# Kernel optimization log

Hardware: AMD Instinct MI355X
Metric: run time of the kernel (lower is better)

Reference implementation:

```python
import jax, jax.numpy as jnp
import numpy as np

T = 2048
D_IN = 1024
D_OUT = 1024
N_HEAD = 16
HEAD_DIM = D_OUT // N_HEAD


def setup_inputs() -> dict:
    key = jax.random.key(0)
    kx, kq, kk, kv = jax.random.split(key, 4)
    s = 1.0 / np.sqrt(D_IN)
    return {
        "x": jax.random.normal(kx, (T, D_IN), dtype=jnp.float32),
        "W_q": jax.random.normal(kq, (D_OUT, D_IN), dtype=jnp.float32) * s,
        "W_k": jax.random.normal(kk, (D_OUT, D_IN), dtype=jnp.float32) * s,
        "W_v": jax.random.normal(kv, (D_OUT, D_IN), dtype=jnp.float32) * s,
    }


def reference(x, W_q, W_k, W_v):
    t = x.shape[0]
    # linear projections (torch Linear: y = x @ W.T), split into heads: [H, T, Dh]
    q = (x @ W_q.T).reshape(t, N_HEAD, HEAD_DIM).transpose(1, 0, 2)
    k = (x @ W_k.T).reshape(t, N_HEAD, HEAD_DIM).transpose(1, 0, 2)
    v = (x @ W_v.T).reshape(t, N_HEAD, HEAD_DIM).transpose(1, 0, 2)
    # raw scores [H, T, T]
    omega = jnp.einsum("hqd,hkd->hqk", q, k)
    causal = jnp.triu(jnp.ones((t, t), dtype=bool), k=1)
    omega = jnp.where(causal[None, :, :], -jnp.inf, omega)
    # NOTE: faithful to source quirk — divides by head_dim**(-0.5),
    # i.e. multiplies scores by sqrt(head_dim)
    att_w = jax.nn.softmax(omega * (HEAD_DIM ** 0.5), axis=-1)
    context = jnp.einsum("hqk,hkd->hqd", att_w, v)  # [H, T, Dh]
    return context.transpose(1, 0, 2).reshape(t, D_OUT)
```

## Files before the change

kernel.cpp:

```cpp
#include <hip/hip_runtime.h>
#include <hip/hip_bf16.h>


typedef __bf16 bf16x8 __attribute__((ext_vector_type(8)));
typedef __bf16 bf16x4 __attribute__((ext_vector_type(4)));
typedef float  f32x4  __attribute__((ext_vector_type(4)));
typedef float  f32x16 __attribute__((ext_vector_type(16)));
typedef unsigned int u32;
typedef u32 u32x2 __attribute__((ext_vector_type(2)));
typedef u32 u32x4 __attribute__((ext_vector_type(4)));

#define MFMA(a, b, c) __builtin_amdgcn_mfma_f32_16x16x32_bf16((a), (b), (c), 0, 0, 0)
#define MFMA32(a, b, c) __builtin_amdgcn_mfma_f32_32x32x16_bf16((a), (b), (c), 0, 0, 0)

#if __has_builtin(__builtin_amdgcn_exp2f)
#define EXP2F(x) __builtin_amdgcn_exp2f(x)
#else
#define EXP2F(x) exp2f(x)
#endif

constexpr int T = 2048, DIN = 1024, DOUT = 1024, NH = 16, DH = 64;
constexpr float SC = 11.5415603f;
constexpr float DEFER = 0.6931472f;

constexpr size_t SZ_XMAT = (size_t)T * DIN * 2;
constexpr size_t SZ_WMAT = (size_t)DOUT * DIN * 2;
constexpr size_t OFF_XH = 0;
constexpr size_t OFF_XL = OFF_XH + SZ_XMAT;
constexpr size_t OFF_QH = OFF_XL + SZ_XMAT;
constexpr size_t OFF_QL = OFF_QH + SZ_XMAT;
constexpr size_t OFF_KH = OFF_QL + SZ_XMAT;
constexpr size_t OFF_KL = OFF_KH + SZ_XMAT;
constexpr size_t OFF_VT = OFF_KL + SZ_XMAT;
constexpr size_t OFF_W  = OFF_VT + SZ_XMAT;

__device__ __forceinline__ void gload_lds16(const void* g, void* l) {
  __builtin_amdgcn_global_load_lds(
      (const __attribute__((address_space(1))) void*)g,
      (__attribute__((address_space(3))) void*)l, 16, 0, 0);
}

__device__ __forceinline__ float xor32f(float x, int hi) {
#if __has_builtin(__builtin_amdgcn_permlane32_swap)
  const u32 xu = __builtin_bit_cast(u32, x);
  const u32x2 rp = __builtin_amdgcn_permlane32_swap(xu, xu, false, false);
  return __builtin_bit_cast(float, hi ? rp[0] : rp[1]);
#else
  return __shfl_xor(x, 32, 64);
#endif
}

__global__ void split_all(const float* __restrict__ x, const float* __restrict__ wq,
                          const float* __restrict__ wk, const float* __restrict__ wv,
                          char* __restrict__ ws) {
  const int i = blockIdx.x * 256 + threadIdx.x;
  const float* src;
  __bf16 *hi, *lo;
  int off;
  if (i < T * DIN / 4) {
    src = x; off = i;
    hi = (__bf16*)(ws + OFF_XH);
    lo = (__bf16*)(ws + OFF_XL);
  } else {
    const int j = i - T * DIN / 4;
    const int z = j >> 18;
    off = j & 262143;
    src = (z == 0) ? wq : ((z == 1) ? wk : wv);
    hi = (__bf16*)(ws + OFF_W + (size_t)z * 2 * SZ_WMAT);
    lo = hi + (size_t)DOUT * DIN;
  }
  const f32x4 v = ((const f32x4*)src)[off];
  bf16x4 h, l;
#pragma unroll
  for (int j = 0; j < 4; ++j) {
    const float xv = v[j];
    const __bf16 hh = (__bf16)xv;
    h[j] = hh;
    l[j] = (__bf16)(xv - (float)hh);
  }
  ((bf16x4*)hi)[off] = h;
  ((bf16x4*)lo)[off] = l;
}

__device__ __forceinline__ void proj_loop_qk(const __bf16* __restrict__ Ah,
                                             const __bf16* __restrict__ Al,
                                             const __bf16* __restrict__ Bh,
                                             const __bf16* __restrict__ Bl,
                                             __bf16* lds, int tm, int tn, int lane,
                                             int wv, f32x4 (&acc)[4][4]) {
  constexpr int BUF = 16384, BOFF = 8192;
  const int wm = wv >> 1, wn = wv & 1;
  const int q4 = lane >> 4, r16 = lane & 15;

  auto STAGE = [&](int ks, int buf) {
    const int k0 = ks * 32;
    __bf16* base = lds + buf * BUF;
#pragma unroll
    for (int j = 0; j < 2; ++j) {
      const int cbase = wv * 128 + j * 64;
      const int cidx = cbase + lane;
      const int row = cidx & 127, kc = cidx >> 7;
      const size_t ga = (size_t)(tm + row) * DIN + k0 + kc * 8;
      const size_t gb = (size_t)(tn + row) * DIN + k0 + kc * 8;
      gload_lds16(Ah + ga, base + cbase * 8);
      gload_lds16(Bh + gb, base + BOFF + cbase * 8);
      gload_lds16(Al + ga, base + 4096 + cbase * 8);
      gload_lds16(Bl + gb, base + 12288 + cbase * 8);
    }
  };

  STAGE(0, 0);
  STAGE(1, 1);

  for (int ks = 0; ks < 32; ++ks) {
    const int buf = ks & 1;
    if (ks < 31) asm volatile("s_waitcnt vmcnt(8)" ::: "memory");
    else         asm volatile("s_waitcnt vmcnt(0)" ::: "memory");
// ... 71 lines not shown
        }
  } else {
    const int vt = bid - 256;
    const int tm = (vt >> 3) * 64;
    const int tn = (vt & 7) * 128;
    const __bf16* Bh = (const __bf16*)(ws + OFF_W + 2 * 2 * SZ_WMAT);

    auto STAGE = [&](int ks, int buf) {
      const int k0 = ks * 32;
      __bf16* base = lds + buf * 6144;
      {
        const int cbase = wv * 64;
        const int c = cbase + lane;
        const int row = c & 63, kc = c >> 6;
        gload_lds16(Ah + (size_t)(tm + row) * DIN + k0 + kc * 8, base + cbase * 8);
      }
#pragma unroll
      for (int j = 0; j < 2; ++j) {
        const int cbase = wv * 128 + j * 64;
        const int c = cbase + lane;
        const int row = c & 127, kc = c >> 7;
        gload_lds16(Bh + (size_t)(tn + row) * DIN + k0 + kc * 8,
                    base + 2048 + cbase * 8);
      }
    };

    f32x4 acc[4][2] = {};
    STAGE(0, 0);
    STAGE(1, 1);
    for (int ks = 0; ks < 32; ++ks) {
      const int buf = ks & 1;
      if (ks < 31) asm volatile("s_waitcnt vmcnt(3)" ::: "memory");
      else         asm volatile("s_waitcnt vmcnt(0)" ::: "memory");
      __builtin_amdgcn_s_barrier();
      __builtin_amdgcn_sched_barrier(0);

      const __bf16* ldsA = lds + buf * 6144;
      const __bf16* ldsB = ldsA + 2048;
      bf16x8 fa[4], fb[2];
#pragma unroll
      for (int b = 0; b < 4; ++b)
        fa[b] = *(const bf16x8*)(ldsA + (q4 * 64 + b * 16 + r16) * 8);
#pragma unroll
      for (int b = 0; b < 2; ++b)
        fb[b] = *(const bf16x8*)(ldsB + (q4 * 128 + wv * 32 + b * 16 + r16) * 8);
      __builtin_amdgcn_s_setprio(1);
#pragma unroll
      for (int bm = 0; bm < 4; ++bm)
#pragma unroll
        for (int bn = 0; bn < 2; ++bn)
          acc[bm][bn] = MFMA(fa[bm], fb[bn], acc[bm][bn]);
      __builtin_amdgcn_s_setprio(0);
      asm volatile("s_waitcnt lgkmcnt(0)" ::: "memory");
      __builtin_amdgcn_sched_barrier(0);
      __builtin_amdgcn_s_barrier();
      __builtin_amdgcn_sched_barrier(0);
      if (ks < 30) STAGE(ks + 2, buf);
    }

    __syncthreads();
    __bf16* tb = lds;
#pragma unroll
    for (int bm = 0; bm < 4; ++bm)
#pragma unroll
      for (int bn = 0; bn < 2; ++bn)
#pragma unroll
        for (int r = 0; r < 4; ++r) {
          const int tl = bm * 16 + q4 * 4 + r;
          const int nl = wv * 32 + bn * 16 + r16;
          tb[(size_t)nl * 72 + tl] = (__bf16)acc[bm][bn][r];
        }
    __syncthreads();
    __bf16* Vt = (__bf16*)(ws + OFF_VT);
#pragma unroll
    for (int it = 0; it < 4; ++it) {
      const int cid = it * 256 + tid;
      const int nl = cid >> 3, tc = cid & 7;
      const bf16x8 vd = *(const bf16x8*)(tb + (size_t)nl * 72 + tc * 8);
      *(bf16x8*)(Vt + (size_t)(tn + nl) * T + tm + tc * 8) = vd;
    }
  }
}

__global__ __launch_bounds__(256, 2) void attn_kernel(const char* __restrict__ ws,
                                                      float* __restrict__ out) {
  const int bid = blockIdx.x;
  const int h = bid & 15;
  const int qt = (bid < 256) ? (31 - (bid >> 4)) : ((bid - 256) >> 4);
  const int tid = threadIdx.x;
  const int lane = tid & 63, wid = tid >> 6;
  const int qhalf = wid & 1, kvpar = wid >> 1;
  const int r32 = lane & 31, hi = lane >> 5, hi8 = hi * 8;
  const int qg = qt * 64 + qhalf * 32 + r32;
  const int NT = qt + 1;
  const int mid = (NT + 1) >> 1;
  const int tBeg = kvpar ? mid : 0;
  const int tEnd = kvpar ? NT : mid;

  const __bf16* Qh = (const __bf16*)(ws + OFF_QH);
  const __bf16* Ql = (const __bf16*)(ws + OFF_QL);
  const __bf16* Kh = (const __bf16*)(ws + OFF_KH);
  const __bf16* Kl = (const __bf16*)(ws + OFF_KL);
  const __bf16* Vt = (const __bf16*)(ws + OFF_VT);

  __shared__ alignas(16) __bf16 sK[2][2][2][64 * 72];

  bf16x8 fqh[4], fql[4];
#pragma unroll
  for (int ds = 0; ds < 4; ++ds) {
    const size_t off = (size_t)qg * DOUT + h * 64 + ds * 16 + hi8;
    fqh[ds] = *(const bf16x8*)(Qh + off);
    fql[ds] = *(const bf16x8*)(Ql + off);
  }

  bf16x8 st[8];
  const int hid = qhalf * 64 + lane;
  auto ISSUE = [&](int t) {
    const int kv0 = t * 64;
#pragma unroll
    for (int j = 0; j < 4; ++j) {
      const int c = j * 128 + hid;
      const int row = c >> 3, dc = c & 7;
      const size_t ko = (size_t)(kv0 + row) * DOUT + h * 64 + dc * 8;
      st[j] = *(const bf16x8*)(Kh + ko);
      st[4 + j] = *(const bf16x8*)(Kl + ko);
    }
  };
  auto WRITE = [&](int b) {
#pragma unroll
    for (int j = 0; j < 4; ++j) {
      const int c = j * 128 + hid;
      const int row = c >> 3, dc = c & 7;
      *(bf16x8*)(&sK[kvpar][b][0][row * 72 + dc * 8]) = st[j];
      *(bf16x8*)(&sK[kvpar][b][1][row * 72 + dc * 8]) = st[4 + j];
    }
  };

  f32x16 acc0 = {}, acc1 = {};
  float mrun = -1e30f, lrun = 0.f;

  if (tBeg < tEnd) {
    ISSUE(tBeg);
    WRITE(0);
    if (tBeg + 1 < tEnd) ISSUE(tBeg + 1);
  }
  asm volatile("s_waitcnt lgkmcnt(0)" ::: "memory");
  __builtin_amdgcn_sched_barrier(0);
  __builtin_amdgcn_s_barrier();
  __builtin_amdgcn_sched_barrier(0);

  for (int it = 0; it < mid; ++it) {
    const int t = tBeg + it;
    const int p = it & 1;
    if (t < tEnd) {
      if (t + 1 < tEnd) {
        WRITE(p ^ 1);
        if (t + 2 < tEnd) ISSUE(t + 2);
      }

      const int kv0 = t * 64;
      const bool dodiag = (t == NT - 1);
      const bool do1 = !(dodiag && qhalf == 0);

      bf16x8 va0[4], va1[4];
#pragma unroll
      for (int ks = 0; ks < 4; ++ks) {
        const size_t vo = (size_t)(h * 64 + r32) * T + kv0 + ks * 16 + hi8;
        va0[ks] = *(const bf16x8*)(Vt + vo);
        va1[ks] = *(const bf16x8*)(Vt + vo + (size_t)32 * T);
      }

      const __bf16* kbh = &sK[kvpar][p][0][0];
      const __bf16* kbl = &sK[kvpar][p][1][0];
      f32x16 s0 = {}, s1 = {};
      __builtin_amdgcn_s_setprio(1);
#pragma unroll
      for (int ds = 0; ds < 4; ++ds) {
        const int ko = ds * 16 + hi8;
        const bf16x8 kh0 = *(const bf16x8*)(kbh + r32 * 72 + ko);
        const bf16x8 kl0 = *(const bf16x8*)(kbl + r32 * 72 + ko);
        s0 = MFMA32(kh0, fqh[ds], s0);
        s0 = MFMA32(kl0, fqh[ds], s0);
        s0 = MFMA32(kh0, fql[ds], s0);
      }
      if (do1) {
#pragma unroll
        for (int ds = 0; ds < 4; ++ds) {
          const int ko = ds * 16 + hi8;
          const bf16x8 kh1 = *(const bf16x8*)(kbh + (32 + r32) * 72 + ko);
          const bf16x8 kl1 = *(const bf16x8*)(kbl + (32 + r32) * 72 + ko);
          s1 = MFMA32(kh1, fqh[ds], s1);
          s1 = MFMA32(kl1, fqh[ds], s1);
          s1 = MFMA32(kh1, fql[ds], s1);
        }
      }
      __builtin_amdgcn_s_setprio(0);

      if (dodiag) {
#pragma unroll
        for (int r = 0; r < 16; ++r) {
          const int kr = (r & 3) + 8 * (r >> 2) + 4 * hi;
          if (kv0 + kr > qg) s0[r] = -1e30f;
          if (kv0 + 32 + kr > qg) s1[r] = -1e30f;
        }
      }

      float mx = -1e30f;
#pragma unroll
      for (int r = 0; r < 16; ++r) {
        mx = fmaxf(mx, s0[r]);
        mx = fmaxf(mx, s1[r]);
      }
      mx = fmaxf(mx, xor32f(mx, hi));

      if (__any(mx - mrun > DEFER)) {
        const float mnew = fmaxf(mrun, mx);
        const float scale = EXP2F((mrun - mnew) * SC);
        mrun = mnew;
        lrun *= scale;
#pragma unroll
        for (int r = 0; r < 16; ++r) {
          acc0[r] *= scale;
          acc1[r] *= scale;
        }
      }
      const float mn2 = mrun * SC;

      float ps = 0.f;
#pragma unroll
      for (int r = 0; r < 16; ++r) {
        s0[r] = EXP2F(__builtin_fmaf(s0[r], SC, -mn2));
        s1[r] = EXP2F(__builtin_fmaf(s1[r], SC, -mn2));
        ps += s0[r] + s1[r];
      }
      ps += xor32f(ps, hi);
      lrun += ps;

      bf16x8 pb[4];
#pragma unroll
      for (int ks = 0; ks < 4; ++ks) {
        const int rb = (ks & 1) * 8;
        bf16x4 lo4, hi4;
#pragma unroll
        for (int j = 0; j < 4; ++j) {
          const float pl = (ks < 2) ? s0[rb + j] : s1[rb + j];
          const float ph = (ks < 2) ? s0[rb + 4 + j] : s1[rb + 4 + j];
          lo4[j] = (__bf16)pl;
          hi4[j] = (__bf16)ph;
        }
        const u32x2 L = __builtin_bit_cast(u32x2, lo4);
        const u32x2 H = __builtin_bit_cast(u32x2, hi4);
        u32x4 f;
#if __has_builtin(__builtin_amdgcn_permlane32_swap)
#pragma unroll
        for (int q = 0; q < 2; ++q) {
          const u32x2 rp = __builtin_amdgcn_permlane32_swap(L[q], H[q], false, false);
          f[q] = rp[0];
          f[2 + q] = rp[1];
        }
#else
#pragma unroll
        for (int q = 0; q < 2; ++q) {
          const u32 send = hi ? L[q] : H[q];
          const u32 recv = (u32)__shfl_xor((int)send, 32, 64);
          f[q] = hi ? recv : L[q];
          f[2 + q] = hi ? H[q] : recv;
        }
#endif
        pb[ks] = __builtin_bit_cast(bf16x8, f);
      }

      __builtin_amdgcn_s_setprio(1);
#pragma unroll
      for (int ks = 0; ks < 4; ++ks) {
        acc0 = MFMA32(va0[ks], pb[ks], acc0);
        acc1 = MFMA32(va1[ks], pb[ks], acc1);
      }
      __builtin_amdgcn_s_setprio(0);
    }

    asm volatile("s_waitcnt lgkmcnt(0)" ::: "memory");
    __builtin_amdgcn_sched_barrier(0);
    __builtin_amdgcn_s_barrier();
    __builtin_amdgcn_sched_barrier(0);
  }

  float* mg = (float*)&sK[0][0][0][0];
  if (kvpar == 1) {
    float* p = mg + (qhalf * 64 + lane) * 34;
    p[0] = mrun;
    p[1] = lrun;
#pragma unroll
    for (int r = 0; r < 16; ++r) {
      p[2 + r] = acc0[r];
      p[18 + r] = acc1[r];
    }
  }
  asm volatile("s_waitcnt lgkmcnt(0)" ::: "memory");
  __builtin_amdgcn_s_barrier();
  if (kvpar == 0) {
    const float* p = mg + (qhalf * 64 + lane) * 34;
    const float m1 = p[0], l1 = p[1];
    const float M = fmaxf(mrun, m1);
    const float w0 = EXP2F((mrun - M) * SC);
    const float w1 = EXP2F((m1 - M) * SC);
    const float rl = 1.0f / (lrun * w0 + l1 * w1);
#pragma unroll
    for (int r = 0; r < 16; ++r) {
      const int d = (r & 3) + 8 * (r >> 2) + 4 * hi;
      out[(size_t)qg * DOUT + h * 64 + d] = (acc0[r] * w0 + p[2 + r] * w1) * rl;
      out[(size_t)qg * DOUT + h * 64 + 32 + d] = (acc1[r] * w0 + p[18 + r] * w1) * rl;
    }
  }
}

extern "C" void kernel_launch(void* const* d_in, const int* in_sizes, int n_in,
                              void* d_out, int out_size, void* d_ws, size_t ws_size,
                              hipStream_t stream) {
  const float* x  = (const float*)d_in[0];
  const float* Wq = (const float*)d_in[1];
  const float* Wk = (const float*)d_in[2];
  const float* Wv = (const float*)d_in[3];
  char* ws = (char*)d_ws;

  split_all<<<5120, 256, 0, stream>>>(x, Wq, Wk, Wv, ws);
  qkv_proj<<<512, 256, 0, stream>>>(ws);
  attn_kernel<<<512, 256, 0, stream>>>(ws, (float*)d_out);
}
```

Measured before the change: 95.21 us.

## Split attention KV range across two blocks and merge partials in a separate kernel

The attention kernel becomes a split-KV partial kernel launched with twice as many blocks. Each block handles half of the causal KV tiles and writes unnormalized partial outputs plus max/sum statistics to workspace. A new merge kernel then combines the two halves and normalizes. The LDS K buffer drops from double to single buffering with an extra barrier per iteration, and launch bounds rise to 4 blocks per CU. The goal is better occupancy and load balance, at the cost of an extra launch, partial-output traffic through memory, and less overlap between K loads and compute.

After: 171.7 us. 1.8x slower.

```diff
diff --git a/kernel.cpp b/kernel.cpp
--- a/kernel.cpp
+++ b/kernel.cpp
@@ -33,6 +33,9 @@
 constexpr size_t OFF_KL = OFF_KH + SZ_XMAT;
 constexpr size_t OFF_VT = OFF_KL + SZ_XMAT;
 constexpr size_t OFF_W  = OFF_VT + SZ_XMAT;
+constexpr size_t OFF_P0 = OFF_XH;
+constexpr size_t OFF_P1 = OFF_W;
+constexpr size_t OFF_ML = OFF_W + ((size_t)8 << 20);
 
 __device__ __forceinline__ void gload_lds16(const void* g, void* l) {
   __builtin_amdgcn_global_load_lds(
@@ -270,9 +273,11 @@
   }
 }
 
-__global__ __launch_bounds__(256, 2) void attn_kernel(const char* __restrict__ ws,
-                                                      float* __restrict__ out) {
-  const int bid = blockIdx.x;
+__global__ __launch_bounds__(256, 4) void attn_part(const char* __restrict__ ws,
+                                                    char* __restrict__ wso) {
+  const int bid0 = blockIdx.x;
+  const int kvhalf = bid0 >> 9;
+  const int bid = bid0 & 511;
   const int h = bid & 15;
   const int qt = (bid < 256) ? (31 - (bid >> 4)) : ((bid - 256) >> 4);
   const int tid = threadIdx.x;
@@ -281,9 +286,13 @@
   const int r32 = lane & 31, hi = lane >> 5, hi8 = hi * 8;
   const int qg = qt * 64 + qhalf * 32 + r32;
   const int NT = qt + 1;
-  const int mid = (NT + 1) >> 1;
-  const int tBeg = kvpar ? mid : 0;
-  const int tEnd = kvpar ? NT : mid;
+  const int midNT = (NT + 1) >> 1;
+  const int rb = kvhalf ? midNT : 0;
+  const int re = kvhalf ? NT : midNT;
+  const int n = re - rb;
+  const int iters = (n + 1) >> 1;
+  const int tBeg = kvpar ? (rb + iters) : rb;
+  const int tEnd = kvpar ? re : (rb + iters);
 
   const __bf16* Qh = (const __bf16*)(ws + OFF_QH);
   const __bf16* Ql = (const __bf16*)(ws + OFF_QL);
@@ -291,7 +300,7 @@
   const __bf16* Kl = (const __bf16*)(ws + OFF_KL);
   const __bf16* Vt = (const __bf16*)(ws + OFF_VT);
 
-  __shared__ alignas(16) __bf16 sK[2][2][2][64 * 72];
+  __shared__ alignas(16) __bf16 sK[2][2][64 * 72];
 
   bf16x8 fqh[4], fql[4];
 #pragma unroll
@@ -314,166 +323,157 @@
       st[4 + j] = *(const bf16x8*)(Kl + ko);
     }
   };
-  auto WRITE = [&](int b) {
+  auto WRITE = [&]() {
 #pragma unroll
     for (int j = 0; j < 4; ++j) {
       const int c = j * 128 + hid;
       const int row = c >> 3, dc = c & 7;
-      *(bf16x8*)(&sK[kvpar][b][0][row * 72 + dc * 8]) = st[j];
-      *(bf16x8*)(&sK[kvpar][b][1][row * 72 + dc * 8]) = st[4 + j];
+      *(bf16x8*)(&sK[kvpar][0][row * 72 + dc * 8]) = st[j];
+      *(bf16x8*)(&sK[kvpar][1][row * 72 + dc * 8]) = st[4 + j];
     }
   };
 
   f32x16 acc0 = {}, acc1 = {};
   float mrun = -1e30f, lrun = 0.f;
 
-  if (tBeg < tEnd) {
-    ISSUE(tBeg);
-    WRITE(0);
-    if (tBeg + 1 < tEnd) ISSUE(tBeg + 1);
-  }
-  asm volatile("s_waitcnt lgkmcnt(0)" ::: "memory");
-  __builtin_amdgcn_sched_barrier(0);
-  __builtin_amdgcn_s_barrier();
-  __builtin_amdgcn_sched_barrier(0);
-
-  for (int it = 0; it < mid; ++it) {
+  if (tBeg < tEnd) ISSUE(tBeg);
+
+  for (int it = 0; it < iters; ++it) {
     const int t = tBeg + it;
-    const int p = it & 1;
-    if (t < tEnd) {
-      if (t + 1 < tEnd) {
-        WRITE(p ^ 1);
-        if (t + 2 < tEnd) ISSUE(t + 2);
-      }
-
-      const int kv0 = t * 64;
-      const bool dodiag = (t == NT - 1);
-      const bool do1 = !(dodiag && qhalf == 0);
-
-      bf16x8 va0[4], va1[4];
-#pragma unroll
-      for (int ks = 0; ks < 4; ++ks) {
-        const size_t vo = (size_t)(h * 64 + r32) * T + kv0 + ks * 16 + hi8;
-        va0[ks] = *(const bf16x8*)(Vt + vo);
-        va1[ks] = *(const bf16x8*)(Vt + vo + (size_t)32 * T);
-      }
-
-      const __bf16* kbh = &sK[kvpar][p][0][0];
-      const __bf16* kbl = &sK[kvpar][p][1][0];
-      f32x16 s0 = {}, s1 = {};
-      __builtin_amdgcn_s_setprio(1);
-#pragma unroll
-      for (int ds = 0; ds < 4; ++ds) {
-        const int ko = ds * 16 + hi8;
-        const bf16x8 kh0 = *(const bf16x8*)(kbh + r32 * 72 + ko);
-        const bf16x8 kl0 = *(const bf16x8*)(kbl + r32 * 72 + ko);
-        s0 = MFMA32(kh0, fqh[ds], s0);
-        s0 = MFMA32(kl0, fqh[ds], s0);
-        s0 = MFMA32(kh0, fql[ds], s0);
-      }
-      if (do1) {
-#pragma unroll
-        for (int ds = 0; ds < 4; ++ds) {
-          const int ko = ds * 16 + hi8;
-          const bf16x8 kh1 = *(const bf16x8*)(kbh + (32 + r32) * 72 + ko);
-          const bf16x8 kl1 = *(const bf16x8*)(kbl + (32 + r32) * 72 + ko);
-          s1 = MFMA32(kh1, fqh[ds], s1);
-          s1 = MFMA32(kl1, fqh[ds], s1);
-          s1 = MFMA32(kh1, fql[ds], s1);
-        }
-      }
-      __builtin_amdgcn_s_setprio(0);
-
-      if (dodiag) {
-#pragma unroll
-        for (int r = 0; r < 16; ++r) {
-          const int kr = (r & 3) + 8 * (r >> 2) + 4 * hi;
-          if (kv0 + kr > qg) s0[r] = -1e30f;
-          if (kv0 + 32 + kr > qg) s1[r] = -1e30f;
-        }
-      }
-
-      float mx = -1e30f;
-#pragma unroll
-      for (int r = 0; r < 16; ++r) {
-        mx = fmaxf(mx, s0[r]);
-        mx = fmaxf(mx, s1[r]);
-      }
-      mx = fmaxf(mx, xor32f(mx, hi));
-
-      if (__any(mx - mrun > DEFER)) {
-        const float mnew = fmaxf(mrun, mx);
-        const float scale = EXP2F((mrun - mnew) * SC);
-        mrun = mnew;
-        lrun *= scale;
-#pragma unroll
-        for (int r = 0; r < 16; ++r) {
-          acc0[r] *= scale;
-          acc1[r] *= scale;
-        }
-      }
-      const float mn2 = mrun * SC;
-
-      float ps = 0.f;
-#pragma unroll
-      for (int r = 0; r < 16; ++r) {
-        s0[r] = EXP2F(__builtin_fmaf(s0[r], SC, -mn2));
-        s1[r] = EXP2F(__builtin_fmaf(s1[r], SC, -mn2));
-        ps += s0[r] + s1[r];
-      }
-      ps += xor32f(ps, hi);
-      lrun += ps;
-
-      bf16x8 pb[4];
-#pragma unroll
-      for (int ks = 0; ks < 4; ++ks) {
-        const int rb = (ks & 1) * 8;
-        bf16x4 lo4, hi4;
-#pragma unroll
-        for (int j = 0; j < 4; ++j) {
-          const float pl = (ks < 2) ? s0[rb + j] : s1[rb + j];
-          const float ph = (ks < 2) ? s0[rb + 4 + j] : s1[rb + 4 + j];
-          lo4[j] = (__bf16)pl;
-          hi4[j] = (__bf16)ph;
-        }
-        const u32x2 L = __builtin_bit_cast(u32x2, lo4);
-        const u32x2 H = __builtin_bit_cast(u32x2, hi4);
-        u32x4 f;
-#if __has_builtin(__builtin_amdgcn_permlane32_swap)
-#pragma unroll
-        for (int q = 0; q < 2; ++q) {
-          const u32x2 rp = __builtin_amdgcn_permlane32_swap(L[q], H[q], false, false);
-          f[q] = rp[0];
-          f[2 + q] = rp[1];
-        }
-#else
-#pragma unroll
-        for (int q = 0; q < 2; ++q) {
-          const u32 send = hi ? L[q] : H[q];
-          const u32 recv = (u32)__shfl_xor((int)send, 32, 64);
-          f[q] = hi ? recv : L[q];
-          f[2 + q] = hi ? H[q] : recv;
-        }
-#endif
-        pb[ks] = __builtin_bit_cast(bf16x8, f);
-      }
-
-      __builtin_amdgcn_s_setprio(1);
-#pragma unroll
-      for (int ks = 0; ks < 4; ++ks) {
-        acc0 = MFMA32(va0[ks], pb[ks], acc0);
-        acc1 = MFMA32(va1[ks], pb[ks], acc1);
-      }
-      __builtin_amdgcn_s_setprio(0);
-    }
-
+    const bool act = (t < tEnd);
+    __builtin_amdgcn_s_barrier();
+    if (act) {
+      WRITE();
+      if (t + 1 < tEnd) ISSUE(t + 1);
+    }
     asm volatile("s_waitcnt lgkmcnt(0)" ::: "memory");
     __builtin_amdgcn_sched_barrier(0);
     __builtin_amdgcn_s_barrier();
-    __builtin_amdgcn_sched_barrier(0);
-  }
-
-  float* mg = (float*)&sK[0][0][0][0];
+    if (!act) continue;
+
+    const int kv0 = t * 64;
+    const bool dodiag = (t == NT - 1);
+    const bool do1 = !(dodiag && qhalf == 0);
+
+    bf16x8 va0[4], va1[4];
+#pragma unroll
+    for (int ks = 0; ks < 4; ++ks) {
+      const size_t vo = (size_t)(h * 64 + r32) * T + kv0 + ks * 16 + hi8;
+      va0[ks] = *(const bf16x8*)(Vt + vo);
+      va1[ks] = *(const bf16x8*)(Vt + vo + (size_t)32 * T);
+    }
+
+    const __bf16* kbh = &sK[kvpar][0][0];
+    const __bf16* kbl = &sK[kvpar][1][0];
+    f32x16 s0 = {}, s1 = {};
+    __builtin_amdgcn_s_setprio(1);
+#pragma unroll
+    for (int ds = 0; ds < 4; ++ds) {
+      const int ko = ds * 16 + hi8;
+      const bf16x8 kh0 = *(const bf16x8*)(kbh + r32 * 72 + ko);
+      const bf16x8 kl0 = *(const bf16x8*)(kbl + r32 * 72 + ko);
+      s0 = MFMA32(kh0, fqh[ds], s0);
+      s0 = MFMA32(kl0, fqh[ds], s0);
+      s0 = MFMA32(kh0, fql[ds], s0);
+    }
+    if (do1) {
+#pragma unroll
+      for (int ds = 0; ds < 4; ++ds) {
+        const int ko = ds * 16 + hi8;
+        const bf16x8 kh1 = *(const bf16x8*)(kbh + (32 + r32) * 72 + ko);
+        const bf16x8 kl1 = *(const bf16x8*)(kbl + (32 + r32) * 72 + ko);
+        s1 = MFMA32(kh1, fqh[ds], s1);
+        s1 = MFMA32(kl1, fqh[ds], s1);
+        s1 = MFMA32(kh1, fql[ds], s1);
+      }
+    }
+    __builtin_amdgcn_s_setprio(0);
+
+    if (dodiag) {
+#pragma unroll
+      for (int r = 0; r < 16; ++r) {
+        const int kr = (r & 3) + 8 * (r >> 2) + 4 * hi;
+        if (kv0 + kr > qg) s0[r] = -1e30f;
+        if (kv0 + 32 + kr > qg) s1[r] = -1e30f;
+      }
+    }
+
+    float mx = -1e30f;
+#pragma unroll
+    for (int r = 0; r < 16; ++r) {
+      mx = fmaxf(mx, s0[r]);
+      mx = fmaxf(mx, s1[r]);
+    }
+    mx = fmaxf(mx, xor32f(mx, hi));
+
+    if (__any(mx - mrun > DEFER)) {
+      const float mnew = fmaxf(mrun, mx);
+      const float scale = EXP2F((mrun - mnew) * SC);
+      mrun = mnew;
+      lrun *= scale;
+#pragma unroll
+      for (int r = 0; r < 16; ++r) {
+        acc0[r] *= scale;
+        acc1[r] *= scale;
+      }
+    }
+    const float mn2 = mrun * SC;
+
+    float ps = 0.f;
+#pragma unroll
+    for (int r = 0; r < 16; ++r) {
+      s0[r] = EXP2F(__builtin_fmaf(s0[r], SC, -mn2));
+      s1[r] = EXP2F(__builtin_fmaf(s1[r], SC, -mn2));
+      ps += s0[r] + s1[r];
+    }
+    ps += xor32f(ps, hi);
+    lrun += ps;
+
+    bf16x8 pb[4];
+#pragma unroll
+    for (int ks = 0; ks < 4; ++ks) {
+      const int rb2 = (ks & 1) * 8;
+      bf16x4 lo4, hi4;
+#pragma unroll
+      for (int j = 0; j < 4; ++j) {
+        const float pl = (ks < 2) ? s0[rb2 + j] : s1[rb2 + j];
+        const float ph = (ks < 2) ? s0[rb2 + 4 + j] : s1[rb2 + 4 + j];
+        lo4[j] = (__bf16)pl;
+        hi4[j] = (__bf16)ph;
+      }
+      const u32x2 L = __builtin_bit_cast(u32x2, lo4);
+      const u32x2 H = __builtin_bit_cast(u32x2, hi4);
+      u32x4 f;
+#if __has_builtin(__builtin_amdgcn_permlane32_swap)
+#pragma unroll
+      for (int q = 0; q < 2; ++q) {
+        const u32x2 rp = __builtin_amdgcn_permlane32_swap(L[q], H[q], false, false);
+        f[q] = rp[0];
+        f[2 + q] = rp[1];
+      }
+#else
+#pragma unroll
+      for (int q = 0; q < 2; ++q) {
+        const u32 send = hi ? L[q] : H[q];
+        const u32 recv = (u32)__shfl_xor((int)send, 32, 64);
+        f[q] = hi ? recv : L[q];
+        f[2 + q] = hi ? H[q] : recv;
+      }
+#endif
+      pb[ks] = __builtin_bit_cast(bf16x8, f);
+    }
+
+    __builtin_amdgcn_s_setprio(1);
+#pragma unroll
+    for (int ks = 0; ks < 4; ++ks) {
+      acc0 = MFMA32(va0[ks], pb[ks], acc0);
+      acc1 = MFMA32(va1[ks], pb[ks], acc1);
+    }
+    __builtin_amdgcn_s_setprio(0);
+  }
+
+  __builtin_amdgcn_s_barrier();
+  float* mg = (float*)&sK[0][0][0];
   if (kvpar == 1) {
     float* p = mg + (qhalf * 64 + lane) * 34;
     p[0] = mrun;
@@ -492,14 +492,42 @@
     const float M = fmaxf(mrun, m1);
     const float w0 = EXP2F((mrun - M) * SC);
     const float w1 = EXP2F((m1 - M) * SC);
-    const float rl = 1.0f / (lrun * w0 + l1 * w1);
+    const float L = lrun * w0 + l1 * w1;
+    float* Op = (float*)(wso + (kvhalf ? OFF_P1 : OFF_P0));
 #pragma unroll
     for (int r = 0; r < 16; ++r) {
       const int d = (r & 3) + 8 * (r >> 2) + 4 * hi;
-      out[(size_t)qg * DOUT + h * 64 + d] = (acc0[r] * w0 + p[2 + r] * w1) * rl;
-      out[(size_t)qg * DOUT + h * 64 + 32 + d] = (acc1[r] * w0 + p[18 + r] * w1) * rl;
-    }
-  }
+      Op[(size_t)qg * DOUT + h * 64 + d] = acc0[r] * w0 + p[2 + r] * w1;
+      Op[(size_t)qg * DOUT + h * 64 + 32 + d] = acc1[r] * w0 + p[18 + r] * w1;
+    }
+    if (hi == 0) {
+      float* ml = (float*)(wso + OFF_ML) + ((size_t)kvhalf * 32768 + qg * 16 + h) * 2;
+      ml[0] = M;
+      ml[1] = L;
+    }
+  }
+}
+
+__global__ void attn_merge(const char* __restrict__ ws, float* __restrict__ out) {
+  const int g = blockIdx.x * 256 + threadIdx.x;
+  const int f = g * 4;
+  const int q = f >> 10;
+  const int h = (f & 1023) >> 6;
+  const float* ml = (const float*)(ws + OFF_ML);
+  const float m0 = ml[((size_t)q * 16 + h) * 2 + 0];
+  const float L0 = ml[((size_t)q * 16 + h) * 2 + 1];
+  const float m1 = ml[((size_t)32768 + q * 16 + h) * 2 + 0];
+  const float L1 = ml[((size_t)32768 + q * 16 + h) * 2 + 1];
+  const float M = fmaxf(m0, m1);
+  const float w0 = EXP2F((m0 - M) * SC);
+  const float w1 = EXP2F((m1 - M) * SC);
+  const float rden = 1.0f / (L0 * w0 + L1 * w1);
+  const f32x4 a = ((const f32x4*)(ws + OFF_P0))[g];
+  const f32x4 b = ((const f32x4*)(ws + OFF_P1))[g];
+  f32x4 o;
+#pragma unroll
+  for (int j = 0; j < 4; ++j) o[j] = (a[j] * w0 + b[j] * w1) * rden;
+  ((f32x4*)out)[g] = o;
 }
 
 extern "C" void kernel_launch(void* const* d_in, const int* in_sizes, int n_in,
@@ -513,5 +541,6 @@
 
   split_all<<<5120, 256, 0, stream>>>(x, Wq, Wk, Wv, ws);
   qkv_proj<<<512, 256, 0, stream>>>(ws);
-  attn_kernel<<<512, 256, 0, stream>>>(ws, (float*)d_out);
-}
+  attn_part<<<1024, 256, 0, stream>>>(ws, ws);
+  attn_merge<<<2048, 256, 0, stream>>>(ws, (float*)d_out);
+}
```

## Software-pipeline QK of next tile with softmax and PV of current tile

Applied to the files above, without the earlier changes.

Restructures the flash-attention inner loop so the QK^T MFMAs for tile t+1 are issued before the softmax and PV work of tile t, using ping-pong score registers and a loop unrolled by two. The goal is to overlap the MFMA and transcendental/VALU phases within a wave and hide the LDS latency of the K tile reads. The K double-buffer schedule shifts so WRITE/ISSUE now prefetch tile t+2/t+3, and holding an extra set of score accumulators raises register pressure, which may reduce occupancy.

After: 94.02 us (median of 2 runs). No clear change (-1.2%).

```diff
diff --git a/kernel.cpp b/kernel.cpp
--- a/kernel.cpp
+++ b/kernel.cpp
@@ -327,6 +327,131 @@
   f32x16 acc0 = {}, acc1 = {};
   float mrun = -1e30f, lrun = 0.f;
 
+  auto QK = [&](int p, bool d1, f32x16& o0, f32x16& o1) {
+    const __bf16* kbh = &sK[kvpar][p][0][0];
+    const __bf16* kbl = &sK[kvpar][p][1][0];
+    f32x16 a0 = {}, a1 = {};
+    __builtin_amdgcn_s_setprio(1);
+#pragma unroll
+    for (int ds = 0; ds < 4; ++ds) {
+      const int ko = ds * 16 + hi8;
+      const bf16x8 kh0 = *(const bf16x8*)(kbh + r32 * 72 + ko);
+      const bf16x8 kl0 = *(const bf16x8*)(kbl + r32 * 72 + ko);
+      a0 = MFMA32(kh0, fqh[ds], a0);
+      a0 = MFMA32(kl0, fqh[ds], a0);
+      a0 = MFMA32(kh0, fql[ds], a0);
+    }
+    if (d1) {
+#pragma unroll
+      for (int ds = 0; ds < 4; ++ds) {
+        const int ko = ds * 16 + hi8;
+        const bf16x8 kh1 = *(const bf16x8*)(kbh + (32 + r32) * 72 + ko);
+        const bf16x8 kl1 = *(const bf16x8*)(kbl + (32 + r32) * 72 + ko);
+        a1 = MFMA32(kh1, fqh[ds], a1);
+        a1 = MFMA32(kl1, fqh[ds], a1);
+        a1 = MFMA32(kh1, fql[ds], a1);
+      }
+    }
+    __builtin_amdgcn_s_setprio(0);
+    o0 = a0;
+    o1 = a1;
+  };
+
+  auto SMPV = [&](int t, f32x16& s0, f32x16& s1) {
+    const int kv0 = t * 64;
+    const bool dodiag = (t == NT - 1);
+
+    bf16x8 va0[4], va1[4];
+#pragma unroll
+    for (int ks = 0; ks < 4; ++ks) {
+      const size_t vo = (size_t)(h * 64 + r32) * T + kv0 + ks * 16 + hi8;
+      va0[ks] = *(const bf16x8*)(Vt + vo);
+      va1[ks] = *(const bf16x8*)(Vt + vo + (size_t)32 * T);
+    }
+
+    if (dodiag) {
+#pragma unroll
+      for (int r = 0; r < 16; ++r) {
+        const int kr = (r & 3) + 8 * (r >> 2) + 4 * hi;
+        if (kv0 + kr > qg) s0[r] = -1e30f;
+        if (kv0 + 32 + kr > qg) s1[r] = -1e30f;
+      }
+    }
+
+    float mx = -1e30f;
+#pragma unroll
+    for (int r = 0; r < 16; ++r) {
+      mx = fmaxf(mx, s0[r]);
+      mx = fmaxf(mx, s1[r]);
+    }
+    mx = fmaxf(mx, xor32f(mx, hi));
+
+    if (__any(mx - mrun > DEFER)) {
+      const float mnew = fmaxf(mrun, mx);
+      const float scale = EXP2F((mrun - mnew) * SC);
+      mrun = mnew;
+      lrun *= scale;
+#pragma unroll
+      for (int r = 0; r < 16; ++r) {
+        acc0[r] *= scale;
+        acc1[r] *= scale;
+      }
+    }
+    const float mn2 = mrun * SC;
+
+    float ps = 0.f;
+#pragma unroll
+    for (int r = 0; r < 16; ++r) {
+      s0[r] = EXP2F(__builtin_fmaf(s0[r], SC, -mn2));
+      s1[r] = EXP2F(__builtin_fmaf(s1[r], SC, -mn2));
+      ps += s0[r] + s1[r];
+    }
+    ps += xor32f(ps, hi);
+    lrun += ps;
+
+    bf16x8 pb[4];
+#pragma unroll
+    for (int ks = 0; ks < 4; ++ks) {
+      const int rb = (ks & 1) * 8;
+      bf16x4 lo4, hi4;
+#pragma unroll
+      for (int j = 0; j < 4; ++j) {
+        const float pl = (ks < 2) ? s0[rb + j] : s1[rb + j];
+        const float ph = (ks < 2) ? s0[rb + 4 + j] : s1[rb + 4 + j];
+        lo4[j] = (__bf16)pl;
+        hi4[j] = (__bf16)ph;
+      }
+      const u32x2 L = __builtin_bit_cast(u32x2, lo4);
+      const u32x2 H = __builtin_bit_cast(u32x2, hi4);
+      u32x4 f;
+#if __has_builtin(__builtin_amdgcn_permlane32_swap)
+#pragma unroll
+      for (int q = 0; q < 2; ++q) {
+        const u32x2 rp = __builtin_amdgcn_permlane32_swap(L[q], H[q], false, false);
+        f[q] = rp[0];
+        f[2 + q] = rp[1];
+      }
+#else
+#pragma unroll
+      for (int q = 0; q < 2; ++q) {
+        const u32 send = hi ? L[q] : H[q];
+        const u32 recv = (u32)__shfl_xor((int)send, 32, 64);
+        f[q] = hi ? recv : L[q];
+        f[2 + q] = hi ? H[q] : recv;
+      }
+#endif
+      pb[ks] = __builtin_bit_cast(bf16x8, f);
+    }
+
+    __builtin_amdgcn_s_setprio(1);
+#pragma unroll
+    for (int ks = 0; ks < 4; ++ks) {
+      acc0 = MFMA32(va0[ks], pb[ks], acc0);
+      acc1 = MFMA32(va1[ks], pb[ks], acc1);
+    }
+    __builtin_amdgcn_s_setprio(0);
+  };
+
   if (tBeg < tEnd) {
     ISSUE(tBeg);
     WRITE(0);
@@ -337,140 +462,37 @@
   __builtin_amdgcn_s_barrier();
   __builtin_amdgcn_sched_barrier(0);
 
-  for (int it = 0; it < mid; ++it) {
-    const int t = tBeg + it;
-    const int p = it & 1;
-    if (t < tEnd) {
-      if (t + 1 < tEnd) {
-        WRITE(p ^ 1);
-        if (t + 2 < tEnd) ISSUE(t + 2);
-      }
-
-      const int kv0 = t * 64;
-      const bool dodiag = (t == NT - 1);
-      const bool do1 = !(dodiag && qhalf == 0);
-
-      bf16x8 va0[4], va1[4];
-#pragma unroll
-      for (int ks = 0; ks < 4; ++ks) {
-        const size_t vo = (size_t)(h * 64 + r32) * T + kv0 + ks * 16 + hi8;
-        va0[ks] = *(const bf16x8*)(Vt + vo);
-        va1[ks] = *(const bf16x8*)(Vt + vo + (size_t)32 * T);
-      }
-
-      const __bf16* kbh = &sK[kvpar][p][0][0];
-      const __bf16* kbl = &sK[kvpar][p][1][0];
-      f32x16 s0 = {}, s1 = {};
-      __builtin_amdgcn_s_setprio(1);
-#pragma unroll
-      for (int ds = 0; ds < 4; ++ds) {
-        const int ko = ds * 16 + hi8;
-        const bf16x8 kh0 = *(const bf16x8*)(kbh + r32 * 72 + ko);
-        const bf16x8 kl0 = *(const bf16x8*)(kbl + r32 * 72 + ko);
-        s0 = MFMA32(kh0, fqh[ds], s0);
-        s0 = MFMA32(kl0, fqh[ds], s0);
-        s0 = MFMA32(kh0, fql[ds], s0);
-      }
-      if (do1) {
-#pragma unroll
-        for (int ds = 0; ds < 4; ++ds) {
-          const int ko = ds * 16 + hi8;
-          const bf16x8 kh1 = *(const bf16x8*)(kbh + (32 + r32) * 72 + ko);
-          const bf16x8 kl1 = *(const bf16x8*)(kbl + (32 + r32) * 72 + ko);
-          s1 = MFMA32(kh1, fqh[ds], s1);
-          s1 = MFMA32(kl1, fqh[ds], s1);
-          s1 = MFMA32(kh1, fql[ds], s1);
-        }
-      }
-      __builtin_amdgcn_s_setprio(0);
-
-      if (dodiag) {
-#pragma unroll
-        for (int r = 0; r < 16; ++r) {
-          const int kr = (r & 3) + 8 * (r >> 2) + 4 * hi;
-          if (kv0 + kr > qg) s0[r] = -1e30f;
-          if (kv0 + 32 + kr > qg) s1[r] = -1e30f;
-        }
-      }
-
-      float mx = -1e30f;
-#pragma unroll
-      for (int r = 0; r < 16; ++r) {
-        mx = fmaxf(mx, s0[r]);
-        mx = fmaxf(mx, s1[r]);
-      }
-      mx = fmaxf(mx, xor32f(mx, hi));
-
-      if (__any(mx - mrun > DEFER)) {
-        const float mnew = fmaxf(mrun, mx);
-        const float scale = EXP2F((mrun - mnew) * SC);
-        mrun = mnew;
-        lrun *= scale;
-#pragma unroll
-        for (int r = 0; r < 16; ++r) {
-          acc0[r] *= scale;
-          acc1[r] *= scale;
-        }
-      }
-      const float mn2 = mrun * SC;
-
-      float ps = 0.f;
-#pragma unroll
-      for (int r = 0; r < 16; ++r) {
-        s0[r] = EXP2F(__builtin_fmaf(s0[r], SC, -mn2));
-        s1[r] = EXP2F(__builtin_fmaf(s1[r], SC, -mn2));
-        ps += s0[r] + s1[r];
-      }
-      ps += xor32f(ps, hi);
-      lrun += ps;
-
-      bf16x8 pb[4];
-#pragma unroll
-      for (int ks = 0; ks < 4; ++ks) {
-        const int rb = (ks & 1) * 8;
-        bf16x4 lo4, hi4;
-#pragma unroll
-        for (int j = 0; j < 4; ++j) {
-          const float pl = (ks < 2) ? s0[rb + j] : s1[rb + j];
-          const float ph = (ks < 2) ? s0[rb + 4 + j] : s1[rb + 4 + j];
-          lo4[j] = (__bf16)pl;
-          hi4[j] = (__bf16)ph;
-        }
-        const u32x2 L = __builtin_bit_cast(u32x2, lo4);
-        const u32x2 H = __builtin_bit_cast(u32x2, hi4);
-        u32x4 f;
-#if __has_builtin(__builtin_amdgcn_permlane32_swap)
-#pragma unroll
-        for (int q = 0; q < 2; ++q) {
-          const u32x2 rp = __builtin_amdgcn_permlane32_swap(L[q], H[q], false, false);
-          f[q] = rp[0];
-          f[2 + q] = rp[1];
-        }
-#else
-#pragma unroll
-        for (int q = 0; q < 2; ++q) {
-          const u32 send = hi ? L[q] : H[q];
-          const u32 recv = (u32)__shfl_xor((int)send, 32, 64);
-          f[q] = hi ? recv : L[q];
-          f[2 + q] = hi ? H[q] : recv;
-        }
-#endif
-        pb[ks] = __builtin_bit_cast(bf16x8, f);
-      }
-
-      __builtin_amdgcn_s_setprio(1);
-#pragma unroll
-      for (int ks = 0; ks < 4; ++ks) {
-        acc0 = MFMA32(va0[ks], pb[ks], acc0);
-        acc1 = MFMA32(va1[ks], pb[ks], acc1);
-      }
-      __builtin_amdgcn_s_setprio(0);
-    }
-
+  f32x16 sA0 = {}, sA1 = {}, sB0 = {}, sB1 = {};
+  if (tBeg < tEnd) {
+    QK(0, !((tBeg == NT - 1) && qhalf == 0), sA0, sA1);
+    if (tBeg + 1 < tEnd) {
+      WRITE(1);
+      if (tBeg + 2 < tEnd) ISSUE(tBeg + 2);
+    }
+  }
+  asm volatile("s_waitcnt lgkmcnt(0)" ::: "memory");
+  __builtin_amdgcn_sched_barrier(0);
+  __builtin_amdgcn_s_barrier();
+  __builtin_amdgcn_sched_barrier(0);
+
+  auto BODY = [&](int i, f32x16& c0, f32x16& c1, f32x16& n0, f32x16& n1) {
+    const int t = tBeg + i;
+    if (t + 1 < tEnd)
+      QK((i + 1) & 1, !((t + 1 == NT - 1) && qhalf == 0), n0, n1);
+    if (t < tEnd) SMPV(t, c0, c1);
+    if (t + 2 < tEnd) {
+      WRITE(i & 1);
+      if (t + 3 < tEnd) ISSUE(t + 3);
+    }
     asm volatile("s_waitcnt lgkmcnt(0)" ::: "memory");
     __builtin_amdgcn_sched_barrier(0);
     __builtin_amdgcn_s_barrier();
     __builtin_amdgcn_sched_barrier(0);
+  };
+
+  for (int i = 0; i < mid; i += 2) {
+    BODY(i, sA0, sA1, sB0, sB1);
+    BODY(i + 1, sB0, sB1, sA0, sA1);
   }
 
   float* mg = (float*)&sK[0][0][0][0];
```

## Split attention KV range across four waves per 32-query block, drop LDS K staging

Applied to the files above, without the earlier changes.

Restructures the attention kernel so each block handles 32 queries of one head, with the four waves splitting the causal KV range into quarters and merging partial softmax states through shared memory. K tiles are now loaded straight from global into registers with a software double buffer, replacing the LDS-staged K pipeline and its per-iteration barriers. The grid doubles to 1024 blocks and launch bounds ask for 4 blocks per CU to raise occupancy and improve load balance. In exchange, K is re-read from global or L2 by more blocks, register pressure may rise under the tighter launch bound, and the final merge now combines four partial results instead of two.

Result: slower. 228.2 us (+139.7%).

```diff
diff --git a/kernel.cpp b/kernel.cpp
--- a/kernel.cpp
+++ b/kernel.cpp
@@ -270,20 +270,19 @@
   }
 }
 
-__global__ __launch_bounds__(256, 2) void attn_kernel(const char* __restrict__ ws,
+__global__ __launch_bounds__(256, 4) void attn_kernel(const char* __restrict__ ws,
                                                       float* __restrict__ out) {
   const int bid = blockIdx.x;
   const int h = bid & 15;
-  const int qt = (bid < 256) ? (31 - (bid >> 4)) : ((bid - 256) >> 4);
+  const int g = 63 - (bid >> 4);
   const int tid = threadIdx.x;
-  const int lane = tid & 63, wid = tid >> 6;
-  const int qhalf = wid & 1, kvpar = wid >> 1;
+  const int wid = tid >> 6, lane = tid & 63;
   const int r32 = lane & 31, hi = lane >> 5, hi8 = hi * 8;
-  const int qg = qt * 64 + qhalf * 32 + r32;
-  const int NT = qt + 1;
-  const int mid = (NT + 1) >> 1;
-  const int tBeg = kvpar ? mid : 0;
-  const int tEnd = kvpar ? NT : mid;
+  const int qg = g * 32 + r32;
+  const int NT = (g >> 1) + 1;
+  const int len = (NT + 3) >> 2;
+  const int tBeg = wid * len;
+  const int tEnd = (tBeg + len < NT) ? (tBeg + len) : NT;
 
   const __bf16* Qh = (const __bf16*)(ws + OFF_QH);
   const __bf16* Ql = (const __bf16*)(ws + OFF_QL);
@@ -291,7 +290,7 @@
   const __bf16* Kl = (const __bf16*)(ws + OFF_KL);
   const __bf16* Vt = (const __bf16*)(ws + OFF_VT);
 
-  __shared__ alignas(16) __bf16 sK[2][2][2][64 * 72];
+  __shared__ float mg[3][64][34];
 
   bf16x8 fqh[4], fql[4];
 #pragma unroll
@@ -301,181 +300,152 @@
     fql[ds] = *(const bf16x8*)(Ql + off);
   }
 
-  bf16x8 st[8];
-  const int hid = qhalf * 64 + lane;
-  auto ISSUE = [&](int t) {
-    const int kv0 = t * 64;
-#pragma unroll
-    for (int j = 0; j < 4; ++j) {
-      const int c = j * 128 + hid;
-      const int row = c >> 3, dc = c & 7;
-      const size_t ko = (size_t)(kv0 + row) * DOUT + h * 64 + dc * 8;
-      st[j] = *(const bf16x8*)(Kh + ko);
-      st[4 + j] = *(const bf16x8*)(Kl + ko);
-    }
-  };
-  auto WRITE = [&](int b) {
-#pragma unroll
-    for (int j = 0; j < 4; ++j) {
-      const int c = j * 128 + hid;
-      const int row = c >> 3, dc = c & 7;
-      *(bf16x8*)(&sK[kvpar][b][0][row * 72 + dc * 8]) = st[j];
-      *(bf16x8*)(&sK[kvpar][b][1][row * 72 + dc * 8]) = st[4 + j];
-    }
-  };
-
   f32x16 acc0 = {}, acc1 = {};
   float mrun = -1e30f, lrun = 0.f;
 
+  auto LOADK = [&](int krow0, bf16x8 (&kh)[4], bf16x8 (&kl)[4]) {
+    const __bf16* ph = Kh + (size_t)(krow0 + r32) * DOUT + h * 64 + hi8;
+    const __bf16* pl = Kl + (size_t)(krow0 + r32) * DOUT + h * 64 + hi8;
+#pragma unroll
+    for (int ds = 0; ds < 4; ++ds) {
+      kh[ds] = *(const bf16x8*)(ph + ds * 16);
+      kl[ds] = *(const bf16x8*)(pl + ds * 16);
+    }
+  };
+
+  auto TILE = [&](int t, bf16x8 (&ch)[4], bf16x8 (&cl)[4],
+                  bf16x8 (&nh)[4], bf16x8 (&nl)[4]) {
+    const int kv0 = t * 64;
+    const bool last = (t == NT - 1);
+    const bool do1 = !(last && ((g & 1) == 0));
+
+    bf16x8 dh[4], dl[4];
+    if (do1) LOADK(kv0 + 32, dh, dl);
+
+    bf16x8 va0[4], va1[4];
+#pragma unroll
+    for (int ks = 0; ks < 4; ++ks) {
+      const size_t vo = (size_t)(h * 64 + r32) * T + kv0 + ks * 16 + hi8;
+      va0[ks] = *(const bf16x8*)(Vt + vo);
+      va1[ks] = *(const bf16x8*)(Vt + vo + (size_t)32 * T);
+    }
+
+    f32x16 s0 = {}, s1 = {};
+    __builtin_amdgcn_s_setprio(1);
+#pragma unroll
+    for (int ds = 0; ds < 4; ++ds) {
+      s0 = MFMA32(ch[ds], fqh[ds], s0);
+      s0 = MFMA32(cl[ds], fqh[ds], s0);
+      s0 = MFMA32(ch[ds], fql[ds], s0);
+    }
+    if (do1) {
+#pragma unroll
+      for (int ds = 0; ds < 4; ++ds) {
+        s1 = MFMA32(dh[ds], fqh[ds], s1);
+        s1 = MFMA32(dl[ds], fqh[ds], s1);
+        s1 = MFMA32(dh[ds], fql[ds], s1);
+      }
+    }
+    __builtin_amdgcn_s_setprio(0);
+
+    if (t + 1 < tEnd) LOADK(kv0 + 64, nh, nl);
+
+    if (last) {
+#pragma unroll
+      for (int r = 0; r < 16; ++r) {
+        const int kr = (r & 3) + 8 * (r >> 2) + 4 * hi;
+        if (kv0 + kr > qg) s0[r] = -1e30f;
+        if (kv0 + 32 + kr > qg) s1[r] = -1e30f;
+      }
+    }
+
+    float mx = -1e30f;
+#pragma unroll
+    for (int r = 0; r < 16; ++r) {
+      mx = fmaxf(mx, s0[r]);
+      mx = fmaxf(mx, s1[r]);
+    }
+    mx = fmaxf(mx, xor32f(mx, hi));
+
+    if (__any(mx - mrun > DEFER)) {
+      const float mnew = fmaxf(mrun, mx);
+      const float scale = EXP2F((mrun - mnew) * SC);
+      mrun = mnew;
+      lrun *= scale;
+#pragma unroll
+      for (int r = 0; r < 16; ++r) {
+        acc0[r] *= scale;
+        acc1[r] *= scale;
+      }
+    }
+    const float mn2 = mrun * SC;
+
+    float ps = 0.f;
+#pragma unroll
+    for (int r = 0; r < 16; ++r) {
+      s0[r] = EXP2F(__builtin_fmaf(s0[r], SC, -mn2));
+      s1[r] = EXP2F(__builtin_fmaf(s1[r], SC, -mn2));
+      ps += s0[r] + s1[r];
+    }
+    ps += xor32f(ps, hi);
+    lrun += ps;
+
+    bf16x8 pb[4];
+#pragma unroll
+    for (int ks = 0; ks < 4; ++ks) {
+      const int rb = (ks & 1) * 8;
+      bf16x4 lo4, hi4;
+#pragma unroll
+      for (int j = 0; j < 4; ++j) {
+        const float pl = (ks < 2) ? s0[rb + j] : s1[rb + j];
+        const float ph = (ks < 2) ? s0[rb + 4 + j] : s1[rb + 4 + j];
+        lo4[j] = (__bf16)pl;
+        hi4[j] = (__bf16)ph;
+      }
+      const u32x2 L = __builtin_bit_cast(u32x2, lo4);
+      const u32x2 H = __builtin_bit_cast(u32x2, hi4);
+      u32x4 f;
+#if __has_builtin(__builtin_amdgcn_permlane32_swap)
+#pragma unroll
+      for (int q = 0; q < 2; ++q) {
+        const u32x2 rp = __builtin_amdgcn_permlane32_swap(L[q], H[q], false, false);
+        f[q] = rp[0];
+        f[2 + q] = rp[1];
+      }
+#else
+#pragma unroll
+      for (int q = 0; q < 2; ++q) {
+        const u32 send = hi ? L[q] : H[q];
+        const u32 recv = (u32)__shfl_xor((int)send, 32, 64);
+        f[q] = hi ? recv : L[q];
+        f[2 + q] = hi ? H[q] : recv;
+      }
+#endif
+      pb[ks] = __builtin_bit_cast(bf16x8, f);
+    }
+
+    __builtin_amdgcn_s_setprio(1);
+#pragma unroll
+    for (int ks = 0; ks < 4; ++ks) {
+      acc0 = MFMA32(va0[ks], pb[ks], acc0);
+      acc1 = MFMA32(va1[ks], pb[ks], acc1);
+    }
+    __builtin_amdgcn_s_setprio(0);
+  };
+
+  bf16x8 kAh[4], kAl[4], kBh[4], kBl[4];
   if (tBeg < tEnd) {
-    ISSUE(tBeg);
-    WRITE(0);
-    if (tBeg + 1 < tEnd) ISSUE(tBeg + 1);
-  }
-  asm volatile("s_waitcnt lgkmcnt(0)" ::: "memory");
-  __builtin_amdgcn_sched_barrier(0);
-  __builtin_amdgcn_s_barrier();
-  __builtin_amdgcn_sched_barrier(0);
-
-  for (int it = 0; it < mid; ++it) {
-    const int t = tBeg + it;
-    const int p = it & 1;
-    if (t < tEnd) {
-      if (t + 1 < tEnd) {
-        WRITE(p ^ 1);
-        if (t + 2 < tEnd) ISSUE(t + 2);
-      }
-
-      const int kv0 = t * 64;
-      const bool dodiag = (t == NT - 1);
-      const bool do1 = !(dodiag && qhalf == 0);
-
-      bf16x8 va0[4], va1[4];
-#pragma unroll
-      for (int ks = 0; ks < 4; ++ks) {
-        const size_t vo = (size_t)(h * 64 + r32) * T + kv0 + ks * 16 + hi8;
-        va0[ks] = *(const bf16x8*)(Vt + vo);
-        va1[ks] = *(const bf16x8*)(Vt + vo + (size_t)32 * T);
-      }
-
-      const __bf16* kbh = &sK[kvpar][p][0][0];
-      const __bf16* kbl = &sK[kvpar][p][1][0];
-      f32x16 s0 = {}, s1 = {};
-      __builtin_amdgcn_s_setprio(1);
-#pragma unroll
-      for (int ds = 0; ds < 4; ++ds) {
-        const int ko = ds * 16 + hi8;
-        const bf16x8 kh0 = *(const bf16x8*)(kbh + r32 * 72 + ko);
-        const bf16x8 kl0 = *(const bf16x8*)(kbl + r32 * 72 + ko);
-        s0 = MFMA32(kh0, fqh[ds], s0);
-        s0 = MFMA32(kl0, fqh[ds], s0);
-        s0 = MFMA32(kh0, fql[ds], s0);
-      }
-      if (do1) {
-#pragma unroll
-        for (int ds = 0; ds < 4; ++ds) {
-          const int ko = ds * 16 + hi8;
-          const bf16x8 kh1 = *(const bf16x8*)(kbh + (32 + r32) * 72 + ko);
-          const bf16x8 kl1 = *(const bf16x8*)(kbl + (32 + r32) * 72 + ko);
-          s1 = MFMA32(kh1, fqh[ds], s1);
-          s1 = MFMA32(kl1, fqh[ds], s1);
-          s1 = MFMA32(kh1, fql[ds], s1);
-        }
-      }
-      __builtin_amdgcn_s_setprio(0);
-
-      if (dodiag) {
-#pragma unroll
-        for (int r = 0; r < 16; ++r) {
-          const int kr = (r & 3) + 8 * (r >> 2) + 4 * hi;
-          if (kv0 + kr > qg) s0[r] = -1e30f;
-          if (kv0 + 32 + kr > qg) s1[r] = -1e30f;
-        }
-      }
-
-      float mx = -1e30f;
-#pragma unroll
-      for (int r = 0; r < 16; ++r) {
-        mx = fmaxf(mx, s0[r]);
-        mx = fmaxf(mx, s1[r]);
-      }
-      mx = fmaxf(mx, xor32f(mx, hi));
-
-      if (__any(mx - mrun > DEFER)) {
-        const float mnew = fmaxf(mrun, mx);
-        const float scale = EXP2F((mrun - mnew) * SC);
-        mrun = mnew;
-        lrun *= scale;
-#pragma unroll
-        for (int r = 0; r < 16; ++r) {
-          acc0[r] *= scale;
-          acc1[r] *= scale;
-        }
-      }
-      const float mn2 = mrun * SC;
-
-      float ps = 0.f;
-#pragma unroll
-      for (int r = 0; r < 16; ++r) {
-        s0[r] = EXP2F(__builtin_fmaf(s0[r], SC, -mn2));
-        s1[r] = EXP2F(__builtin_fmaf(s1[r], SC, -mn2));
-        ps += s0[r] + s1[r];
-      }
-      ps += xor32f(ps, hi);
-      lrun += ps;
-
-      bf16x8 pb[4];
-#pragma unroll
-      for (int ks = 0; ks < 4; ++ks) {
-        const int rb = (ks & 1) * 8;
-        bf16x4 lo4, hi4;
-#pragma unroll
-        for (int j = 0; j < 4; ++j) {
-          const float pl = (ks < 2) ? s0[rb + j] : s1[rb + j];
-          const float ph = (ks < 2) ? s0[rb + 4 + j] : s1[rb + 4 + j];
-          lo4[j] = (__bf16)pl;
-          hi4[j] = (__bf16)ph;
-        }
-        const u32x2 L = __builtin_bit_cast(u32x2, lo4);
-        const u32x2 H = __builtin_bit_cast(u32x2, hi4);
-        u32x4 f;
-#if __has_builtin(__builtin_amdgcn_permlane32_swap)
-#pragma unroll
-        for (int q = 0; q < 2; ++q) {
-          const u32x2 rp = __builtin_amdgcn_permlane32_swap(L[q], H[q], false, false);
-          f[q] = rp[0];
-          f[2 + q] = rp[1];
-        }
-#else
-#pragma unroll
-        for (int q = 0; q < 2; ++q) {
-          const u32 send = hi ? L[q] : H[q];
-          const u32 recv = (u32)__shfl_xor((int)send, 32, 64);
-          f[q] = hi ? recv : L[q];
-          f[2 + q] = hi ? H[q] : recv;
-        }
-#endif
-        pb[ks] = __builtin_bit_cast(bf16x8, f);
-      }
-
-      __builtin_amdgcn_s_setprio(1);
-#pragma unroll
-      for (int ks = 0; ks < 4; ++ks) {
-        acc0 = MFMA32(va0[ks], pb[ks], acc0);
-        acc1 = MFMA32(va1[ks], pb[ks], acc1);
-      }
-      __builtin_amdgcn_s_setprio(0);
-    }
-
-    asm volatile("s_waitcnt lgkmcnt(0)" ::: "memory");
-    __builtin_amdgcn_sched_barrier(0);
-    __builtin_amdgcn_s_barrier();
-    __builtin_amdgcn_sched_barrier(0);
-  }
-
-  float* mg = (float*)&sK[0][0][0][0];
-  if (kvpar == 1) {
-    float* p = mg + (qhalf * 64 + lane) * 34;
+    LOADK(tBeg * 64, kAh, kAl);
+    int t = tBeg;
+    for (; t + 2 <= tEnd; t += 2) {
+      TILE(t, kAh, kAl, kBh, kBl);
+      TILE(t + 1, kBh, kBl, kAh, kAl);
+    }
+    if (t < tEnd) TILE(t, kAh, kAl, kBh, kBl);
+  }
+
+  if (wid > 0) {
+    float* p = &mg[wid - 1][lane][0];
     p[0] = mrun;
     p[1] = lrun;
 #pragma unroll
@@ -486,18 +456,30 @@
   }
   asm volatile("s_waitcnt lgkmcnt(0)" ::: "memory");
   __builtin_amdgcn_s_barrier();
-  if (kvpar == 0) {
-    const float* p = mg + (qhalf * 64 + lane) * 34;
-    const float m1 = p[0], l1 = p[1];
-    const float M = fmaxf(mrun, m1);
+  if (wid == 0) {
+    float M = mrun;
+#pragma unroll
+    for (int s = 0; s < 3; ++s) M = fmaxf(M, mg[s][lane][0]);
     const float w0 = EXP2F((mrun - M) * SC);
-    const float w1 = EXP2F((m1 - M) * SC);
-    const float rl = 1.0f / (lrun * w0 + l1 * w1);
+    float Lt = lrun * w0;
+    f32x16 o0 = acc0 * w0, o1 = acc1 * w0;
+#pragma unroll
+    for (int s = 0; s < 3; ++s) {
+      const float* p = &mg[s][lane][0];
+      const float w = EXP2F((p[0] - M) * SC);
+      Lt += p[1] * w;
+#pragma unroll
+      for (int r = 0; r < 16; ++r) {
+        o0[r] += p[2 + r] * w;
+        o1[r] += p[18 + r] * w;
+      }
+    }
+    const float rl = 1.0f / Lt;
 #pragma unroll
     for (int r = 0; r < 16; ++r) {
       const int d = (r & 3) + 8 * (r >> 2) + 4 * hi;
-      out[(size_t)qg * DOUT + h * 64 + d] = (acc0[r] * w0 + p[2 + r] * w1) * rl;
-      out[(size_t)qg * DOUT + h * 64 + 32 + d] = (acc1[r] * w0 + p[18 + r] * w1) * rl;
+      out[(size_t)qg * DOUT + h * 64 + d] = o0[r] * rl;
+      out[(size_t)qg * DOUT + h * 64 + 32 + d] = o1[r] * rl;
     }
   }
 }
@@ -513,5 +495,5 @@
 
   split_all<<<5120, 256, 0, stream>>>(x, Wq, Wk, Wv, ws);
   qkv_proj<<<512, 256, 0, stream>>>(ws);
-  attn_kernel<<<512, 256, 0, stream>>>(ws, (float*)d_out);
-}
+  attn_kernel<<<1024, 256, 0, stream>>>(ws, (float*)d_out);
+}
```
